# Optimization experiments

Measured on AMD Instinct MI355X. Metric: run time of the kernel, lower is better.

The kernel has to match this reference:

```python
import jax, jax.numpy as jnp
import numpy as np

N, E = 100000, 400000
IN, HID, H, D = 165, 128, 8, 16  # per-head dim D = HID // H
NUM_CLASSES = 2


def layer_norm(x, g, b, eps=1e-5):
    m = jnp.mean(x, axis=-1, keepdims=True)
    v = jnp.var(x, axis=-1, keepdims=True)
    return (x - m) / jnp.sqrt(v + eps) * g + b


def transformer_conv(x, src, dst, Wq, bq, Wk, bk, Wv, bv, Ws, bs):
    # x: [N, HID]; src/dst: [E]
    n = x.shape[0]
    q = (x @ Wq + bq).reshape(n, H, D)
    k = (x @ Wk + bk).reshape(n, H, D)
    v = (x @ Wv + bv).reshape(n, H, D)
    # per-edge attention logits: [E, H]
    alpha = jnp.sum(q[dst] * k[src], axis=-1) / jnp.sqrt(jnp.float32(D))
    # segment softmax over incoming edges of each destination node
    amax = jax.ops.segment_max(alpha, dst, num_segments=n)          # [N, H]
    amax = jnp.where(jnp.isfinite(amax), amax, 0.0)
    ex = jnp.exp(alpha - amax[dst])                                  # [E, H]
    denom = jax.ops.segment_sum(ex, dst, num_segments=n)            # [N, H]
    a = ex / (denom[dst] + 1e-16)
    msg = v[src] * a[..., None]                                      # [E, H, D]
    out = jax.ops.segment_sum(msg, dst, num_segments=n)             # [N, H, D]
    out = out.reshape(n, H * D)
    # root skip connection (root_weight=True, beta=False in PyG defaults)
    return out + x @ Ws + bs


def setup_inputs() -> dict:
    key = jax.random.key(0)
    ks = jax.random.split(key, 24)
    rn = lambda k, s: (jax.random.normal(k, s, jnp.float32) * 0.05)
    inp = {
        "x": jax.random.normal(ks[0], (N, IN), jnp.float32),
        "edge_index": jax.random.randint(ks[1], (2, E), 0, N, jnp.int32),
        "W_in": rn(ks[2], (IN, HID)), "b_in": jnp.zeros((HID,), jnp.float32),
        # layer 1 TransformerConv
        "Wq1": rn(ks[3], (HID, HID)), "bq1": jnp.zeros((HID,), jnp.float32),
        "Wk1": rn(ks[4], (HID, HID)), "bk1": jnp.zeros((HID,), jnp.float32),
        "Wv1": rn(ks[5], (HID, HID)), "bv1": jnp.zeros((HID,), jnp.float32),
        "Ws1": rn(ks[6], (HID, HID)), "bs1": jnp.zeros((HID,), jnp.float32),
        "g1": jnp.ones((HID,), jnp.float32), "be1": jnp.zeros((HID,), jnp.float32),
        # layer 2 TransformerConv
        "Wq2": rn(ks[7], (HID, HID)), "bq2": jnp.zeros((HID,), jnp.float32),
        "Wk2": rn(ks[8], (HID, HID)), "bk2": jnp.zeros((HID,), jnp.float32),
        "Wv2": rn(ks[9], (HID, HID)), "bv2": jnp.zeros((HID,), jnp.float32),
        "Ws2": rn(ks[10], (HID, HID)), "bs2": jnp.zeros((HID,), jnp.float32),
        "g2": jnp.ones((HID,), jnp.float32), "be2": jnp.zeros((HID,), jnp.float32),
        # classifier MLP
        "Wc1": rn(ks[11], (HID, HID // 2)), "bc1": jnp.zeros((HID // 2,), jnp.float32),
        "Wc2": rn(ks[12], (HID // 2, NUM_CLASSES)), "bc2": jnp.zeros((NUM_CLASSES,), jnp.float32),
    }
    return inp


def reference(x, edge_index, W_in, b_in,
              Wq1, bq1, Wk1, bk1, Wv1, bv1, Ws1, bs1, g1, be1,
              Wq2, bq2, Wk2, bk2, Wv2, bv2, Ws2, bs2, g2, be2,
              Wc1, bc1, Wc2, bc2):
    src, dst = edge_index[0], edge_index[1]
    h = x @ W_in + b_in                                   # input projection
    h_new = transformer_conv(h, src, dst, Wq1, bq1, Wk1, bk1, Wv1, bv1, Ws1, bs1)
    h = layer_norm(h + h_new, g1, be1)                    # dropout = identity (eval)
    h_new = transformer_conv(h, src, dst, Wq2, bq2, Wk2, bk2, Wv2, bv2, Ws2, bs2)
    h = layer_norm(h + h_new, g2, be2)
    return jax.nn.relu(h @ Wc1 + bc1) @ Wc2 + bc2         # [N, num_classes]
```

## Files before the change

kernel.cpp:

```cpp
#include <hip/hip_runtime.h>
#include <hip/hip_bf16.h>

#define NN 100000
#define EE 400000
#define IN_DIM 165
#define KPAD 192
#define HID 128
#define C1 64
#define NC 2
#define CAP 32
#define NBD2 782
#define HBLK 1563

typedef const float* fpp;
typedef __hip_bfloat16 bf16;
typedef __attribute__((ext_vector_type(8))) short s16x8;
typedef __attribute__((ext_vector_type(4))) float f32x4;

__device__ __forceinline__ float bflo(unsigned u) { return __uint_as_float(u << 16); }
__device__ __forceinline__ float bfhi(unsigned u) { return __uint_as_float(u & 0xFFFF0000u); }
__device__ __forceinline__ float us2f(unsigned short u) { return __uint_as_float((unsigned)u << 16); }
__device__ __forceinline__ unsigned short bfbits(float f) {
    bf16 h = __float2bfloat16(f);
    return *reinterpret_cast<unsigned short*>(&h);
}

__global__ void k_prep(const int* __restrict__ src, const int* __restrict__ dst,
                       int* __restrict__ deg, int* __restrict__ esrc,
                       fpp W_in, fpp Wq1, fpp Wk1, fpp Wv1, fpp Ws1,
                       fpp Wq2, fpp Wk2, fpp Wv2, fpp Ws2, fpp Wc1,
                       fpp bq1, fpp bk1, fpp bv1, fpp bs1,
                       fpp bq2, fpp bk2, fpp bv2, fpp bs2,
                       unsigned short* __restrict__ winpack,
                       unsigned short* __restrict__ wpack,
                       unsigned short* __restrict__ wc1t,
                       float* __restrict__ bpack) {
    if (blockIdx.x < HBLK) {
        int e = blockIdx.x * 256 + threadIdx.x;
        if (e < EE) {
            int d = dst[e];
            int p = atomicAdd(&deg[d], 1);
            if (p < CAP) esrc[d * CAP + p] = src[e];
        }
        return;
    }
    int idx = (blockIdx.x - HBLK) * 256 + threadIdx.x;
    if (idx < 24576) {
        int n = idx / KPAD, k = idx % KPAD;
        float v = (k < IN_DIM) ? W_in[k * HID + n] : 0.f;
        winpack[idx] = bfbits(v);
    } else if (idx < 155648) {
        int local = idx - 24576;
        int layer = local >> 16;
        int rest = local & 65535;
        int chunk = rest >> 14;
        int l14 = rest & 16383;
        int n = l14 >> 7, k = l14 & 127;
        const float* srcw;
        int col;
        float scale = 1.f;
        if (chunk == 0) { srcw = layer ? Wq2 : Wq1; col = n; scale = 0.25f; }
        else if (chunk == 3) { srcw = layer ? Ws2 : Ws1; col = n; }
        else {
            int a = ((chunk == 2) ? 16 : 0) + (n >> 3), e = n & 7;
            srcw = (e < 4) ? (layer ? Wk2 : Wk1) : (layer ? Wv2 : Wv1);
            col = 4 * a + (e & 3);
        }
        wpack[local] = bfbits(srcw[k * HID + col] * scale);
    } else if (idx < 163840) {
        int local = idx - 155648;
        int n = local >> 7, k = local & 127;
        wc1t[local] = bfbits(Wc1[k * C1 + n]);
    } else if (idx < 164864) {
        int local = idx - 163840;
        int layer = local >> 9;
        int rest = local & 511;
        int chunk = rest >> 7, n = rest & 127;
        const float* srcb;
        int col;
        float scale = 1.f;
        if (chunk == 0) { srcb = layer ? bq2 : bq1; col = n; scale = 0.25f; }
        else if (chunk == 3) { srcb = layer ? bs2 : bs1; col = n; }
        else {
            int a = ((chunk == 2) ? 16 : 0) + (n >> 3), e = n & 7;
            srcb = (e < 4) ? (layer ? bk2 : bk1) : (layer ? bv2 : bv1);
            col = 4 * a + (e & 3);
        }
        bpack[local] = srcb[col] * scale;
    }
}

__global__ __launch_bounds__(256) void k_dense_in(const float* __restrict__ x,
                                                  const unsigned short* __restrict__ winpack,
                                                  fpp b_in, unsigned short* __restrict__ hb) {
    __shared__ unsigned short smem[18432];
    unsigned short* As = smem;
    unsigned short* Ws = smem + 9216;
    int row0 = blockIdx.x * 128;
    int t = threadIdx.x, lane = t & 63, w = t >> 6;
    int quad = lane >> 4, l16 = lane & 15;
    int m_off = (w >> 1) * 64, n_off = (w & 1) * 64;

    f32x4 acc[4][4];
    float bias_v[4];
#pragma unroll
    for (int ni = 0; ni < 4; ni++) bias_v[ni] = b_in[n_off + ni * 16 + l16];
#pragma unroll
    for (int mi = 0; mi < 4; mi++)
#pragma unroll
        for (int ni = 0; ni < 4; ni++)
            acc[mi][ni] = (f32x4){bias_v[ni], bias_v[ni], bias_v[ni], bias_v[ni]};

    for (int kc = 0; kc < 3; kc++) {
        __syncthreads();
        for (int i = 0; i < 4; i++) {
            int g = t + i * 256;
            int r = g >> 3, c = g & 7;
            int rg = min(row0 + r, NN - 1);
            int col0 = kc * 64 + c * 8;
            s16x8 us;
#pragma unroll
            for (int j = 0; j < 8; j++) {
                int col = col0 + j;
                float v = (col < IN_DIM) ? x[(size_t)rg * IN_DIM + col] : 0.f;
                us[j] = (short)bfbits(v);
            }
            *(s16x8*)(As + r * 72 + c * 8) = us;
            *(s16x8*)(Ws + r * 72 + c * 8) = *(const s16x8*)(winpack + r * KPAD + col0);
        }
        __syncthreads();
#pragma unroll
        for (int ks = 0; ks < 2; ks++) {
            int k0 = ks * 32;
            s16x8 a[4], b[4];
#pragma unroll
            for (int mi = 0; mi < 4; mi++)
                a[mi] = *(const s16x8*)(As + (m_off + mi * 16 + l16) * 72 + k0 + quad * 8);
#pragma unroll
            for (int ni = 0; ni < 4; ni++)
                b[ni] = *(const s16x8*)(Ws + (n_off + ni * 16 + l16) * 72 + k0 + quad * 8);
#pragma unroll
            for (int mi = 0; mi < 4; mi++)
#pragma unroll
                for (int ni = 0; ni < 4; ni++)
                    acc[mi][ni] = __builtin_amdgcn_mfma_f32_16x16x32_bf16(
                        a[mi], b[ni], acc[mi][ni], 0, 0, 0);
        }
    }
    __syncthreads();
    unsigned short* Cs = smem;
#pragma unroll
    for (int mi = 0; mi < 4; mi++)
#pragma unroll
        for (int ni = 0; ni < 4; ni++)
#pragma unroll
            for (int r = 0; r < 4; r++)
                Cs[(m_off + mi * 16 + quad * 4 + r) * 136 + n_off + ni * 16 + l16] =
                    bfbits(acc[mi][ni][r]);
    __syncthreads();
    for (int i = 0; i < 8; i++) {
        int g = t + i * 256;
        int r = g >> 4, c = g & 15;
        if (row0 + r < NN)
            *(s16x8*)(hb + (size_t)(row0 + r) * HID + c * 8) =
                *(const s16x8*)(Cs + r * 136 + c * 8);
    }
}

__global__ __launch_bounds__(256) void k_dense4(const unsigned short* __restrict__ hb,
                                                const unsigned short* __restrict__ wpackL,
                                                const float* __restrict__ bpackL,
                                                bf16* __restrict__ qb, bf16* __restrict__ kvb,
                                                bf16* __restrict__ agg) {
    __shared__ unsigned short As[128 * 136];
    __shared__ unsigned short Ws[128 * 136];
    int row0 = blockIdx.x * 128;
    int t = threadIdx.x, lane = t & 63, w = t >> 6;
    int quad = lane >> 4, l16 = lane & 15;
    int m_off = (w >> 1) * 64, n_off = (w & 1) * 64;

    for (int i = 0; i < 8; i++) {
        int g = t + i * 256;
        int r = g >> 4, c = g & 15;
        int rg = min(row0 + r, NN - 1);
        *(s16x8*)(As + r * 136 + c * 8) = *(const s16x8*)(hb + (size_t)rg * HID + c * 8);
    }
    __syncthreads();

    s16x8 afr[4][4];
#pragma unroll
    for (int ks = 0; ks < 4; ks++)
#pragma unroll
        for (int mi = 0; mi < 4; mi++)
            afr[ks][mi] = *(const s16x8*)(As + (m_off + mi * 16 + l16) * 136 + ks * 32 + quad * 8);

    for (int nc = 0; nc < 4; nc++) {
        unsigned short* tp; int stride;
        if (nc == 0)      { tp = (unsigned short*)qb;        stride = 128; }
        else if (nc == 1) { tp = (unsigned short*)kvb;       stride = 256; }
        else if (nc == 2) { tp = (unsigned short*)kvb + 128; stride = 256; }
        else              { tp = (unsigned short*)agg;       stride = 128; }
        const float* bp = bpackL + nc * 128;

        __syncthreads();
        for (int i = 0; i < 8; i++) {
            int g = t + i * 256;
            int r = g >> 4, c = g & 15;
            *(s16x8*)(Ws + r * 136 + c * 8) =
                *(const s16x8*)(wpackL + nc * 16384 + r * HID + c * 8);
        }
        __syncthreads();

        f32x4 acc[4][4];
        float bias_v[4];
#pragma unroll
        for (int ni = 0; ni < 4; ni++) bias_v[ni] = bp[n_off + ni * 16 + l16];
#pragma unroll
        for (int mi = 0; mi < 4; mi++)
#pragma unroll
            for (int ni = 0; ni < 4; ni++)
                acc[mi][ni] = (f32x4){bias_v[ni], bias_v[ni], bias_v[ni], bias_v[ni]};

#pragma unroll
        for (int ks = 0; ks < 4; ks++) {
            s16x8 b[4];
#pragma unroll
            for (int ni = 0; ni < 4; ni++)
                b[ni] = *(const s16x8*)(Ws + (n_off + ni * 16 + l16) * 136 + ks * 32 + quad * 8);
#pragma unroll
            for (int mi = 0; mi < 4; mi++)
#pragma unroll
                for (int ni = 0; ni < 4; ni++)
                    acc[mi][ni] = __builtin_amdgcn_mfma_f32_16x16x32_bf16(
                        afr[ks][mi], b[ni], acc[mi][ni], 0, 0, 0);
        }
        __syncthreads();

        unsigned short* Cs = Ws;
#pragma unroll
        for (int mi = 0; mi < 4; mi++)
#pragma unroll
            for (int ni = 0; ni < 4; ni++)
#pragma unroll
                for (int r = 0; r < 4; r++)
                    Cs[(m_off + mi * 16 + quad * 4 + r) * 136 + n_off + ni * 16 + l16] =
                        bfbits(acc[mi][ni][r]);
        __syncthreads();
        if (nc == 3) {
            for (int i = 0; i < 8; i++) {
                int g = t + i * 256;
                int r = g >> 4, c = g & 15;
                if (row0 + r < NN) {
                    s16x8 cv = *(const s16x8*)(Cs + r * 136 + c * 8);
                    s16x8 hv = *(const s16x8*)(As + r * 136 + c * 8);
                    s16x8 ov;
#pragma unroll
                    for (int j = 0; j < 8; j++)
                        ov[j] = (short)bfbits(us2f((unsigned short)cv[j]) +
                                              us2f((unsigned short)hv[j]));
                    *(s16x8*)(tp + (size_t)(row0 + r) * stride + c * 8) = ov;
                }
            }
        } else {
            for (int i = 0; i < 8; i++) {
                int g = t + i * 256;
                int r = g >> 4, c = g & 15;
                if (row0 + r < NN)
                    *(s16x8*)(tp + (size_t)(row0 + r) * stride + c * 8) =
                        *(const s16x8*)(Cs + r * 136 + c * 8);
            }
        }
    }
}

__global__ void k_agg_ln(const bf16* __restrict__ qb, const bf16* __restrict__ kvb,
                         const int* __restrict__ deg, const int* __restrict__ esrc,
                         const bf16* __restrict__ agg, unsigned short* __restrict__ hb,
                         fpp g, fpp b) {
    int wv = (blockIdx.x * blockDim.x + threadIdx.x) >> 6;
    int lane = threadIdx.x & 63;
    int l32 = lane & 31;
    int d = wv * 2 + (lane >> 5);
    if (d >= NN) return;
    const int* bucket = esrc + d * CAP;
    int cnt = min(deg[d], CAP);
    uint4 i40 = *(const uint4*)bucket;
    uint2 qu = ((const uint2*)(qb + (size_t)d * HID))[l32];
    float q0 = bflo(qu.x), q1 = bfhi(qu.x);
    float q2 = bflo(qu.y), q3 = bfhi(qu.y);
    uint2 au = ((const uint2*)(agg + (size_t)d * HID))[l32];
    float4 gv = ((const float4*)g)[l32];
    float4 bv = ((const float4*)b)[l32];

    uint4 kv[4];
    float tt[4];
    float m = -INFINITY;
#pragma unroll
    for (int j = 0; j < 4; j++) {
        int s = ((const int*)&i40)[j];
        if (j < cnt) kv[j] = ((const uint4*)(kvb + (size_t)s * 256))[l32];
        else kv[j] = (uint4){0u, 0u, 0u, 0u};
        float t = q0 * bflo(kv[j].x) + q1 * bfhi(kv[j].x) +
                  q2 * bflo(kv[j].y) + q3 * bfhi(kv[j].y);
        t += __shfl_xor(t, 1);
        t += __shfl_xor(t, 2);
        tt[j] = (j < cnt) ? t : -INFINITY;
        m = fmaxf(m, tt[j]);
    }
    if (cnt == 0) m = 0.f;
    float L = 0.f, o0 = 0.f, o1 = 0.f, o2 = 0.f, o3 = 0.f;
#pragma unroll
    for (int j = 0; j < 4; j++) {
        float p = __expf(tt[j] - m);
        L += p;
        o0 += p * bflo(kv[j].z);
        o1 += p * bfhi(kv[j].z);
        o2 += p * bflo(kv[j].w);
        o3 += p * bfhi(kv[j].w);
    }

    for (int base = 4; base < cnt; base += 4) {
        uint4 i4 = *(const uint4*)(bucket + base);
#pragma unroll
        for (int j = 0; j < 4; j++) {
            if (base + j < cnt) {
                int s = ((const int*)&i4)[j];
                uint4 kvt = ((const uint4*)(kvb + (size_t)s * 256))[l32];
                float t = q0 * bflo(kvt.x) + q1 * bfhi(kvt.x) +
                          q2 * bflo(kvt.y) + q3 * bfhi(kvt.y);
                t += __shfl_xor(t, 1);
                t += __shfl_xor(t, 2);
                float nm = fmaxf(m, t);
                float corr = __expf(m - nm);
                float p = __expf(t - nm);
                L = L * corr + p;
                o0 = o0 * corr + p * bflo(kvt.z);
                o1 = o1 * corr + p * bfhi(kvt.z);
                o2 = o2 * corr + p * bflo(kvt.w);
                o3 = o3 * corr + p * bfhi(kvt.w);
                m = nm;
            }
        }
    }

    float inv = 1.f / (L + 1e-16f);
    float v0 = bflo(au.x) + o0 * inv;
    float v1 = bfhi(au.x) + o1 * inv;
    float v2 = bflo(au.y) + o2 * inv;
    float v3 = bfhi(au.y) + o3 * inv;
    float s = v0 + v1 + v2 + v3;
    float s2 = v0 * v0 + v1 * v1 + v2 * v2 + v3 * v3;
    for (int off = 16; off; off >>= 1) {
        s += __shfl_xor(s, off);
        s2 += __shfl_xor(s2, off);
    }
    float mn = s * (1.f / HID);
    float var = s2 * (1.f / HID) - mn * mn;
    float invs = rsqrtf(var + 1e-5f);
    float ox = (v0 - mn) * invs * gv.x + bv.x;
    float oy = (v1 - mn) * invs * gv.y + bv.y;
    float oz = (v2 - mn) * invs * gv.z + bv.z;
    float ow = (v3 - mn) * invs * gv.w + bv.w;
    uint2 outw;
    outw.x = ((unsigned)bfbits(oy) << 16) | bfbits(ox);
    outw.y = ((unsigned)bfbits(ow) << 16) | bfbits(oz);
    ((uint2*)(hb + (size_t)d * HID))[l32] = outw;
}

__global__ __launch_bounds__(256) void k_classifier(const unsigned short* __restrict__ hb,
                                                    const unsigned short* __restrict__ wc1t,
                                                    fpp bc1, fpp Wc2, fpp bc2,
                                                    float* __restrict__ out) {
    __shared__ unsigned short As[128 * 136];
    __shared__ unsigned short Ws[64 * 136];
    int row0 = blockIdx.x * 128;
    int t = threadIdx.x, lane = t & 63, w = t >> 6;
    int quad = lane >> 4, l16 = lane & 15;
    int m_off = w * 32;

    for (int i = 0; i < 8; i++) {
        int g = t + i * 256;
        int r = g >> 4, c = g & 15;
        int rg = min(row0 + r, NN - 1);
        *(s16x8*)(As + r * 136 + c * 8) = *(const s16x8*)(hb + (size_t)rg * HID + c * 8);
    }
    for (int i = 0; i < 4; i++) {
        int g = t + i * 256;
        int r = g >> 4, c = g & 15;
        *(s16x8*)(Ws + r * 136 + c * 8) = *(const s16x8*)(wc1t + r * HID + c * 8);
    }
    __syncthreads();

    f32x4 acc[2][4];
    float bias_v[4];
#pragma unroll
    for (int ni = 0; ni < 4; ni++) bias_v[ni] = bc1[ni * 16 + l16];
#pragma unroll
    for (int mi = 0; mi < 2; mi++)
#pragma unroll
        for (int ni = 0; ni < 4; ni++)
            acc[mi][ni] = (f32x4){bias_v[ni], bias_v[ni], bias_v[ni], bias_v[ni]};

#pragma unroll
    for (int ks = 0; ks < 4; ks++) {
        s16x8 a[2], b[4];
#pragma unroll
        for (int mi = 0; mi < 2; mi++)
            a[mi] = *(const s16x8*)(As + (m_off + mi * 16 + l16) * 136 + ks * 32 + quad * 8);
#pragma unroll
        for (int ni = 0; ni < 4; ni++)
            b[ni] = *(const s16x8*)(Ws + (ni * 16 + l16) * 136 + ks * 32 + quad * 8);
#pragma unroll
        for (int mi = 0; mi < 2; mi++)
#pragma unroll
            for (int ni = 0; ni < 4; ni++)
                acc[mi][ni] = __builtin_amdgcn_mfma_f32_16x16x32_bf16(
                    a[mi], b[ni], acc[mi][ni], 0, 0, 0);
    }
    __syncthreads();
    float* Cs = (float*)As;
#pragma unroll
    for (int mi = 0; mi < 2; mi++)
#pragma unroll
        for (int ni = 0; ni < 4; ni++)
#pragma unroll
            for (int r = 0; r < 4; r++)
                Cs[(m_off + mi * 16 + quad * 4 + r) * 68 + ni * 16 + l16] =
                    fmaxf(acc[mi][ni][r], 0.f);
    __syncthreads();

    int row = t >> 1, half = t & 1;
    float p0 = 0.f, p1 = 0.f;
    for (int c = half * 32; c < half * 32 + 32; c++) {
        float v = Cs[row * 68 + c];
        p0 += v * Wc2[c * NC + 0];
        p1 += v * Wc2[c * NC + 1];
    }
    p0 += __shfl_xor(p0, 1, 64);
    p1 += __shfl_xor(p1, 1, 64);
    if (half == 0 && row0 + row < NN) {
        out[(size_t)(row0 + row) * NC + 0] = p0 + bc2[0];
        out[(size_t)(row0 + row) * NC + 1] = p1 + bc2[1];
    }
}

extern "C" void kernel_launch(void* const* d_in, const int* in_sizes, int n_in,
                              void* d_out, int out_size, void* d_ws, size_t ws_size,
                              hipStream_t stream) {
    fpp x = (fpp)d_in[0];
    const int* ei = (const int*)d_in[1];
    const int* src = ei;
    const int* dst = ei + EE;
    fpp W_in = (fpp)d_in[2];  fpp b_in = (fpp)d_in[3];
    fpp Wq1 = (fpp)d_in[4];   fpp bq1 = (fpp)d_in[5];
    fpp Wk1 = (fpp)d_in[6];   fpp bk1 = (fpp)d_in[7];
    fpp Wv1 = (fpp)d_in[8];   fpp bv1 = (fpp)d_in[9];
    fpp Ws1 = (fpp)d_in[10];  fpp bs1 = (fpp)d_in[11];
    fpp g1 = (fpp)d_in[12];   fpp be1 = (fpp)d_in[13];
    fpp Wq2 = (fpp)d_in[14];  fpp bq2 = (fpp)d_in[15];
    fpp Wk2 = (fpp)d_in[16];  fpp bk2 = (fpp)d_in[17];
    fpp Wv2 = (fpp)d_in[18];  fpp bv2 = (fpp)d_in[19];
    fpp Ws2 = (fpp)d_in[20];  fpp bs2 = (fpp)d_in[21];
    fpp g2 = (fpp)d_in[22];   fpp be2 = (fpp)d_in[23];
    fpp Wc1 = (fpp)d_in[24];  fpp bc1 = (fpp)d_in[25];
    fpp Wc2 = (fpp)d_in[26];  fpp bc2 = (fpp)d_in[27];
    float* out = (float*)d_out;

    char* p = (char*)d_ws;
    unsigned short* hb = (unsigned short*)p;  p += (size_t)NN * HID * 2;
    bf16* agg = (bf16*)p;            p += (size_t)NN * HID * 2;
    bf16* qb = (bf16*)p;             p += (size_t)NN * HID * 2;
    bf16* kvb = (bf16*)p;            p += (size_t)NN * 256 * 2;
    int* deg = (int*)p;              p += (size_t)NN * 4;
    int* esrc = (int*)p;             p += (size_t)NN * CAP * 4;
    unsigned short* winpack = (unsigned short*)p;  p += 24576 * 2;
    unsigned short* wpack = (unsigned short*)p;    p += 131072 * 2;
    unsigned short* wc1t = (unsigned short*)p;     p += 8192 * 2;
    float* bpack = (float*)p;                      p += 1024 * 4;

    hipMemsetAsync(deg, 0, (size_t)NN * 4, stream);
    k_prep<<<HBLK + 644, 256, 0, stream>>>(src, dst, deg, esrc,
                                           W_in, Wq1, Wk1, Wv1, Ws1,
                                           Wq2, Wk2, Wv2, Ws2, Wc1,
                                           bq1, bk1, bv1, bs1, bq2, bk2, bv2, bs2,
                                           winpack, wpack, wc1t, bpack);

    k_dense_in<<<NBD2, 256, 0, stream>>>(x, winpack, b_in, hb);

    for (int layer = 0; layer < 2; layer++) {
        fpp g = layer ? g2 : g1, be = layer ? be2 : be1;
        const unsigned short* wpackL = wpack + (size_t)layer * 65536;
        const float* bpackL = bpack + (size_t)layer * 512;

        k_dense4<<<NBD2, 256, 0, stream>>>(hb, wpackL, bpackL, qb, kvb, agg);
        k_agg_ln<<<12500, 256, 0, stream>>>(qb, kvb, deg, esrc, agg, hb, g, be);
    }

    k_classifier<<<NBD2, 256, 0, stream>>>(hb, wc1t, bc1, Wc2, bc2, out);
}
```

Baseline: 370.4 us.

## Read GEMM weight fragments straight from global memory and shrink LDS footprint

The three dense GEMM kernels no longer stage weight tiles in shared memory. Each wave now loads its B fragments directly from global memory, where the small, heavily reused weights should stay cache-resident. k_dense4 also drops the register-held A fragments in favour of per-k-step LDS reads, and writes results back in two 64-row halves so it can use a smaller C staging buffer. Launch-bounds occupancy hints are added to raise the number of resident blocks, at the cost of more global/L2 traffic and extra barriers in the epilogue.

```diff
diff --git a/kernel.cpp b/kernel.cpp
--- a/kernel.cpp
+++ b/kernel.cpp
@@ -90,12 +90,11 @@
     }
 }
 
-__global__ __launch_bounds__(256) void k_dense_in(const float* __restrict__ x,
-                                                  const unsigned short* __restrict__ winpack,
-                                                  fpp b_in, unsigned short* __restrict__ hb) {
-    __shared__ unsigned short smem[18432];
+__global__ __launch_bounds__(256, 4) void k_dense_in(const float* __restrict__ x,
+                                                     const unsigned short* __restrict__ winpack,
+                                                     fpp b_in, unsigned short* __restrict__ hb) {
+    __shared__ unsigned short smem[17408];
     unsigned short* As = smem;
-    unsigned short* Ws = smem + 9216;
     int row0 = blockIdx.x * 128;
     int t = threadIdx.x, lane = t & 63, w = t >> 6;
     int quad = lane >> 4, l16 = lane & 15;
@@ -126,7 +125,6 @@
                 us[j] = (short)bfbits(v);
             }
             *(s16x8*)(As + r * 72 + c * 8) = us;
-            *(s16x8*)(Ws + r * 72 + c * 8) = *(const s16x8*)(winpack + r * KPAD + col0);
         }
         __syncthreads();
 #pragma unroll
@@ -138,7 +136,8 @@
                 a[mi] = *(const s16x8*)(As + (m_off + mi * 16 + l16) * 72 + k0 + quad * 8);
 #pragma unroll
             for (int ni = 0; ni < 4; ni++)
-                b[ni] = *(const s16x8*)(Ws + (n_off + ni * 16 + l16) * 72 + k0 + quad * 8);
+                b[ni] = *(const s16x8*)(winpack + (n_off + ni * 16 + l16) * KPAD +
+                                        kc * 64 + k0 + quad * 8);
 #pragma unroll
             for (int mi = 0; mi < 4; mi++)
 #pragma unroll
@@ -167,13 +166,13 @@
     }
 }
 
-__global__ __launch_bounds__(256) void k_dense4(const unsigned short* __restrict__ hb,
-                                                const unsigned short* __restrict__ wpackL,
-                                                const float* __restrict__ bpackL,
-                                                bf16* __restrict__ qb, bf16* __restrict__ kvb,
-                                                bf16* __restrict__ agg) {
+__global__ __launch_bounds__(256, 3) void k_dense4(const unsigned short* __restrict__ hb,
+                                                   const unsigned short* __restrict__ wpackL,
+                                                   const float* __restrict__ bpackL,
+                                                   bf16* __restrict__ qb, bf16* __restrict__ kvb,
+                                                   bf16* __restrict__ agg) {
     __shared__ unsigned short As[128 * 136];
-    __shared__ unsigned short Ws[128 * 136];
+    __shared__ unsigned short Cs[64 * 136];
     int row0 = blockIdx.x * 128;
     int t = threadIdx.x, lane = t & 63, w = t >> 6;
     int quad = lane >> 4, l16 = lane & 15;
@@ -186,13 +185,6 @@
         *(s16x8*)(As + r * 136 + c * 8) = *(const s16x8*)(hb + (size_t)rg * HID + c * 8);
     }
     __syncthreads();
-
-    s16x8 afr[4][4];
-#pragma unroll
-    for (int ks = 0; ks < 4; ks++)
-#pragma unroll
-        for (int mi = 0; mi < 4; mi++)
-            afr[ks][mi] = *(const s16x8*)(As + (m_off + mi * 16 + l16) * 136 + ks * 32 + quad * 8);
 
     for (int nc = 0; nc < 4; nc++) {
         unsigned short* tp; int stride;
@@ -201,15 +193,7 @@
         else if (nc == 2) { tp = (unsigned short*)kvb + 128; stride = 256; }
         else              { tp = (unsigned short*)agg;       stride = 128; }
         const float* bp = bpackL + nc * 128;
-
-        __syncthreads();
-        for (int i = 0; i < 8; i++) {
-            int g = t + i * 256;
-            int r = g >> 4, c = g & 15;
-            *(s16x8*)(Ws + r * 136 + c * 8) =
-                *(const s16x8*)(wpackL + nc * 16384 + r * HID + c * 8);
-        }
-        __syncthreads();
+        const unsigned short* wb = wpackL + nc * 16384;
 
         f32x4 acc[4][4];
         float bias_v[4];
@@ -223,51 +207,49 @@
 
 #pragma unroll
         for (int ks = 0; ks < 4; ks++) {
-            s16x8 b[4];
+            s16x8 a[4], b[4];
+#pragma unroll
+            for (int mi = 0; mi < 4; mi++)
+                a[mi] = *(const s16x8*)(As + (m_off + mi * 16 + l16) * 136 + ks * 32 + quad * 8);
 #pragma unroll
             for (int ni = 0; ni < 4; ni++)
-                b[ni] = *(const s16x8*)(Ws + (n_off + ni * 16 + l16) * 136 + ks * 32 + quad * 8);
+                b[ni] = *(const s16x8*)(wb + (n_off + ni * 16 + l16) * HID + ks * 32 + quad * 8);
 #pragma unroll
             for (int mi = 0; mi < 4; mi++)
 #pragma unroll
                 for (int ni = 0; ni < 4; ni++)
                     acc[mi][ni] = __builtin_amdgcn_mfma_f32_16x16x32_bf16(
-                        afr[ks][mi], b[ni], acc[mi][ni], 0, 0, 0);
-        }
-        __syncthreads();
-
-        unsigned short* Cs = Ws;
-#pragma unroll
-        for (int mi = 0; mi < 4; mi++)
-#pragma unroll
-            for (int ni = 0; ni < 4; ni++)
-#pragma unroll
-                for (int r = 0; r < 4; r++)
-                    Cs[(m_off + mi * 16 + quad * 4 + r) * 136 + n_off + ni * 16 + l16] =
-                        bfbits(acc[mi][ni][r]);
-        __syncthreads();
-        if (nc == 3) {
-            for (int i = 0; i < 8; i++) {
+                        a[mi], b[ni], acc[mi][ni], 0, 0, 0);
+        }
+
+        for (int hh = 0; hh < 2; hh++) {
+            __syncthreads();
+            if ((w >> 1) == hh) {
+#pragma unroll
+                for (int mi = 0; mi < 4; mi++)
+#pragma unroll
+                    for (int ni = 0; ni < 4; ni++)
+#pragma unroll
+                        for (int r = 0; r < 4; r++)
+                            Cs[(mi * 16 + quad * 4 + r) * 136 + n_off + ni * 16 + l16] =
+                                bfbits(acc[mi][ni][r]);
+            }
+            __syncthreads();
+            for (int i = 0; i < 4; i++) {
                 int g = t + i * 256;
                 int r = g >> 4, c = g & 15;
-                if (row0 + r < NN) {
+                int grow = row0 + hh * 64 + r;
+                if (grow < NN) {
                     s16x8 cv = *(const s16x8*)(Cs + r * 136 + c * 8);
-                    s16x8 hv = *(const s16x8*)(As + r * 136 + c * 8);
-                    s16x8 ov;
-#pragma unroll
-                    for (int j = 0; j < 8; j++)
-                        ov[j] = (short)bfbits(us2f((unsigned short)cv[j]) +
-                                              us2f((unsigned short)hv[j]));
-                    *(s16x8*)(tp + (size_t)(row0 + r) * stride + c * 8) = ov;
+                    if (nc == 3) {
+                        s16x8 hv = *(const s16x8*)(As + (hh * 64 + r) * 136 + c * 8);
+#pragma unroll
+                        for (int j = 0; j < 8; j++)
+                            cv[j] = (short)bfbits(us2f((unsigned short)cv[j]) +
+                                                  us2f((unsigned short)hv[j]));
+                    }
+                    *(s16x8*)(tp + (size_t)grow * stride + c * 8) = cv;
                 }
-            }
-        } else {
-            for (int i = 0; i < 8; i++) {
-                int g = t + i * 256;
-                int r = g >> 4, c = g & 15;
-                if (row0 + r < NN)
-                    *(s16x8*)(tp + (size_t)(row0 + r) * stride + c * 8) =
-                        *(const s16x8*)(Cs + r * 136 + c * 8);
             }
         }
     }
@@ -318,7 +300,6 @@
         o2 += p * bflo(kv[j].w);
         o3 += p * bfhi(kv[j].w);
     }
-
     for (int base = 4; base < cnt; base += 4) {
         uint4 i4 = *(const uint4*)(bucket + base);
 #pragma unroll
@@ -367,12 +348,11 @@
     ((uint2*)(hb + (size_t)d * HID))[l32] = outw;
 }
 
-__global__ __launch_bounds__(256) void k_classifier(const unsigned short* __restrict__ hb,
-                                                    const unsigned short* __restrict__ wc1t,
-                                                    fpp bc1, fpp Wc2, fpp bc2,
-                                                    float* __restrict__ out) {
+__global__ __launch_bounds__(256, 4) void k_classifier(const unsigned short* __restrict__ hb,
+                                                       const unsigned short* __restrict__ wc1t,
+                                                       fpp bc1, fpp Wc2, fpp bc2,
+                                                       float* __restrict__ out) {
     __shared__ unsigned short As[128 * 136];
-    __shared__ unsigned short Ws[64 * 136];
     int row0 = blockIdx.x * 128;
     int t = threadIdx.x, lane = t & 63, w = t >> 6;
     int quad = lane >> 4, l16 = lane & 15;
@@ -384,11 +364,6 @@
         int rg = min(row0 + r, NN - 1);
         *(s16x8*)(As + r * 136 + c * 8) = *(const s16x8*)(hb + (size_t)rg * HID + c * 8);
     }
-    for (int i = 0; i < 4; i++) {
-        int g = t + i * 256;
-        int r = g >> 4, c = g & 15;
-        *(s16x8*)(Ws + r * 136 + c * 8) = *(const s16x8*)(wc1t + r * HID + c * 8);
-    }
     __syncthreads();
 
     f32x4 acc[2][4];
@@ -409,7 +384,7 @@
             a[mi] = *(const s16x8*)(As + (m_off + mi * 16 + l16) * 136 + ks * 32 + quad * 8);
 #pragma unroll
         for (int ni = 0; ni < 4; ni++)
-            b[ni] = *(const s16x8*)(Ws + (ni * 16 + l16) * 136 + ks * 32 + quad * 8);
+            b[ni] = *(const s16x8*)(wc1t + (ni * 16 + l16) * HID + ks * 32 + quad * 8);
 #pragma unroll
         for (int mi = 0; mi < 2; mi++)
 #pragma unroll
```

Result: slower. 409.6 us (+10.6%).
